# Kernel tuning notes

Hardware: AMD Instinct MI355X
Metric: run time of the kernel (lower is better)

The kernel has to match this reference:

```python
import jax, jax.numpy as jnp
import numpy as np

B, L, P, D, RD, M, K = 128, 128, 1024, 128, 128, 64, 4


def _ln(x, g, b):
    m = x.mean(-1, keepdims=True)
    v = ((x - m) ** 2).mean(-1, keepdims=True)
    return (x - m) / jnp.sqrt(v + 1e-5) * g + b


def _mlp2(x, w1, b1, w2, b2):
    return jax.nn.gelu(x @ w1 + b1, approximate=False) @ w2 + b2


def setup_inputs() -> dict:
    key = jax.random.key(0)
    ks = iter(jax.random.split(key, 64))

    def n(sh, s=1.0):
        return jax.random.normal(next(ks), sh, dtype=jnp.float32) * s

    def lin(i, o):
        return n((i, o), 1.0 / np.sqrt(i))

    inp = {}
    inp['l_pos'] = n((B, L, 3), 3.0)
    inp['l_x'] = n((B, L, 8))
    inp['p_pos'] = n((B, P, 3), 3.0)
    inp['p_x'] = n((B, P, 192))
    inp['p_score'] = n((B, P))
    inp['p_rad'] = jax.random.uniform(next(ks), (B, P), dtype=jnp.float32)
    inp['l_typ'] = jax.random.randint(next(ks), (B, L), 0, 256)
    inp['p_typ'] = jax.random.randint(next(ks), (B, P), 0, 256)
    inp['a_idx'] = jax.random.randint(next(ks), (B, M), 0, L)
    inp['b_idx'] = jax.random.randint(next(ks), (B, M), 0, L)
    inp['l_mask'] = jnp.ones((B, L), dtype=bool)
    inp['p_mask'] = jnp.ones((B, P), dtype=bool)
    inp.update(dict(
        le_emb=n((256, D), 0.02), le_w1=lin(8, D), le_b1=jnp.zeros(D), le_w2=lin(D, D), le_b2=jnp.zeros(D),
        le_g=jnp.ones(D), le_lnb=jnp.zeros(D),
        pe_emb=n((256, D), 0.02), pe_w1=lin(192, D), pe_b1=jnp.zeros(D), pe_w2=lin(D, D), pe_b2=jnp.zeros(D),
        ps_w1=lin(1, D), ps_b1=jnp.zeros(D), ps_w2=lin(D, D), ps_b2=jnp.zeros(D),
        pe_g=jnp.ones(D), pe_lnb=jnp.zeros(D),
        projL=lin(D, D), projP=lin(D, D), dustbin_vec=n((D,), 0.02),
        sg_w1=lin(D, D), sg_b1=jnp.zeros(D), sg_w2=lin(D, 1), sg_b2=jnp.zeros(1),
        inv_w1=lin(3, 64), inv_b1=jnp.zeros(64), inv_w2=lin(64, 1), inv_b2=jnp.zeros(1),
        retrL=lin(D, RD), retrP=lin(D, RD)))
    return inp


def _forward(l_pos, l_x, p_pos, p_x, p_score, p_rad,
             l_typ, p_typ, a_idx, b_idx, l_mask, p_mask,
             le_emb, le_w1, le_b1, le_w2, le_b2, le_g, le_lnb,
             pe_emb, pe_w1, pe_b1, pe_w2, pe_b2,
             ps_w1, ps_b1, ps_w2, ps_b2, pe_g, pe_lnb,
             projL, projP, dustbin_vec,
             sg_w1, sg_b1, sg_w2, sg_b2,
             inv_w1, inv_b1, inv_w2, inv_b2, retrL, retrP):
    neg = jnp.finfo(jnp.float32).min
    # encoders + projections
    hL = _ln(_mlp2(l_x, le_w1, le_b1, le_w2, le_b2) + le_emb[l_typ], le_g, le_lnb) @ projL  # [B,L,D]
    hP_pre = (_mlp2(p_x, pe_w1, pe_b1, pe_w2, pe_b2) + pe_emb[p_typ]
              + _mlp2(p_score[..., None], ps_w1, ps_b1, ps_w2, ps_b2))
    hP = _ln(hP_pre, pe_g, pe_lnb) @ projP  # [B,P,D]
    scale = 1.0 / jnp.sqrt(jnp.float32(hL.shape[-1]))
    # masked bipartite cross-attn logits
    logits = jnp.einsum('bld,bpd->blp', hL, hP) * scale
    logits_feat = jnp.where(p_mask[:, None, :], logits, neg)
    logits_feat = jnp.where(l_mask[:, :, None], logits_feat, neg)
    # dustbin log-softmax assignment
    dust = (hL @ dustbin_vec) * scale  # [B,L]
    full = jnp.concatenate([logits_feat, dust[:, :, None]], axis=-1)  # [B,L,P+1]
    full = jnp.where(l_mask[:, :, None], full, neg)
    logW = jax.nn.log_softmax(full, axis=-1)
    W = jnp.exp(logW)
    pm = p_mask.astype(jnp.float32)
    lm = l_mask.astype(jnp.float32)
    denomL = jnp.maximum(lm.sum(1), 1.0)
    Wm = jnp.concatenate([W[:, :, :-1] * pm[:, None, :], W[:, :, -1:]], axis=-1)
    sharp = (Wm.max(-1) * lm).sum(1) / denomL
    neg_ent = -((-(Wm * logW).sum(-1) * lm).sum(1) / denomL)
    # per-pocket-node sigma
    p_sigma = jax.nn.softplus(_mlp2(hP, sg_w1, sg_b1, sg_w2, sg_b2)[..., 0]) + 1e-3 + jnp.maximum(p_rad, 0.0)
    logW_real = logW[:, :, :-1]
    # sampled edge likelihood
    Bn = l_pos.shape[0]
    bi = jnp.arange(Bn)[:, None]
    valid = l_mask[bi, a_idx] & l_mask[bi, b_idx] & (a_idx != b_idx)  # [B,M]
    dist = jnp.linalg.norm(l_pos[bi, a_idx] - l_pos[bi, b_idx], axis=-1)[:, :, None, None]
    _, topj = jax.lax.top_k(logits_feat, K)  # [B,L,K]
    bi3 = jnp.arange(Bn)[:, None, None]
    p_sel = p_pos[bi3, topj]                 # [B,L,K,3]
    sig_sel = p_sigma[bi3, topj]             # [B,L,K]
    lW_top = jnp.take_along_axis(logW_real, topj, axis=2)  # [B,L,K]
    pa, pb = p_sel[bi, a_idx], p_sel[bi, b_idx]            # [B,M,K,3]
    siga, sigb = sig_sel[bi, a_idx], sig_sel[bi, b_idx]    # [B,M,K]
    lwa, lwb = lW_top[bi, a_idx], lW_top[bi, b_idx]
    mu = jnp.linalg.norm(pa[:, :, :, None, :] - pb[:, :, None, :, :], axis=-1)  # [B,M,K,K]
    sigma = jnp.sqrt(siga[:, :, :, None] ** 2 + sigb[:, :, None, :] ** 2 + 1e-6)
    logw_pair = lwa[:, :, :, None] + lwb[:, :, None, :]
    logp = -0.5 * ((dist - mu) / sigma) ** 2 - jnp.log(sigma) - 0.5 * jnp.log(2.0 * jnp.pi)
    logmix = jax.scipy.special.logsumexp(logw_pair + logp, axis=(-2, -1))  # [B,M]
    vp = valid.astype(jnp.float32)
    edge_raw = (logmix * vp).sum(1) / jnp.maximum(vp.sum(1), 1.0)
    edge = jnp.tanh(edge_raw / 5.0)  # edge_scale
    inv_vec = jnp.stack([sharp, neg_ent, edge], axis=1)  # [B,3]
    score_inv_geom = _mlp2(inv_vec, inv_w1, inv_b1, inv_w2, inv_b2)[..., 0]
    # pooled retrieval embeddings
    l_g = (hL * lm[:, :, None]).sum(1) / jnp.maximum(lm.sum(1, keepdims=True), 1.0)
    p_g = (hP * pm[:, :, None]).sum(1) / jnp.maximum(pm.sum(1, keepdims=True), 1.0)

    def _unit(x):
        return x / jnp.maximum(jnp.linalg.norm(x, axis=-1, keepdims=True), 1e-12)

    l_z = _unit(l_g @ retrL)
    p_z = _unit(p_g @ retrP)
    return jnp.concatenate([score_inv_geom[:, None], l_z, p_z], axis=-1)  # [B, 1+2*RD]


def reference(l_pos, l_x, p_pos, p_x, p_score, p_rad,
              l_typ, p_typ, a_idx, b_idx, l_mask, p_mask,
              le_emb, le_w1, le_b1, le_w2, le_b2, le_g, le_lnb,
              pe_emb, pe_w1, pe_b1, pe_w2, pe_b2,
              ps_w1, ps_b1, ps_w2, ps_b2, pe_g, pe_lnb,
              projL, projP, dustbin_vec,
              sg_w1, sg_b1, sg_w2, sg_b2,
              inv_w1, inv_b1, inv_w2, inv_b2, retrL, retrP):
    return _forward(l_pos, l_x, p_pos, p_x, p_score, p_rad,
                    l_typ, p_typ, a_idx, b_idx, l_mask, p_mask,
                    le_emb, le_w1, le_b1, le_w2, le_b2, le_g, le_lnb,
                    pe_emb, pe_w1, pe_b1, pe_w2, pe_b2,
                    ps_w1, ps_b1, ps_w2, ps_b2, pe_g, pe_lnb,
                    projL, projP, dustbin_vec,
                    sg_w1, sg_b1, sg_w2, sg_b2,
                    inv_w1, inv_b1, inv_w2, inv_b2, retrL, retrP)
```

## Files before the change

### kernel.cpp

```cpp
#include <hip/hip_runtime.h>
#include <math.h>

#define B_ 128
#define L_ 128
#define P_ 1024
#define D_ 128
#define M_ 64

typedef __attribute__((ext_vector_type(8))) short bf16x8;
typedef __attribute__((ext_vector_type(4))) float f32x4;

__device__ __forceinline__ float gelu_exact(float x) {
    return 0.5f * x * (1.0f + erff(x * 0.70710678118654752440f));
}
__device__ __forceinline__ float gelu_fast(float x) {
    float y = 0.7978845608028654f * (x + 0.044715f * x * x * x);
    float e = __expf(2.0f * y);
    float t = 1.0f - 2.0f / (e + 1.0f);
    return 0.5f * x * (1.0f + t);
}
__device__ __forceinline__ float softplus_f(float x) {
    return fmaxf(x, 0.0f) + log1pf(expf(-fabsf(x)));
}
__device__ __forceinline__ unsigned short f2bf(float f) {
    unsigned int u = __float_as_uint(f);
    unsigned int r = (u + 0x7FFFu + ((u >> 16) & 1u)) >> 16;
    return (unsigned short)r;
}
__device__ __forceinline__ float bf2f(unsigned short h) {
    return __uint_as_float(((unsigned int)h) << 16);
}
__device__ __forceinline__ bf16x8 pack8(float4 a, float4 b) {
    union { unsigned int u[4]; bf16x8 v; } r;
    r.u[0] = (unsigned)f2bf(a.x) | ((unsigned)f2bf(a.y) << 16);
    r.u[1] = (unsigned)f2bf(a.z) | ((unsigned)f2bf(a.w) << 16);
    r.u[2] = (unsigned)f2bf(b.x) | ((unsigned)f2bf(b.y) << 16);
    r.u[3] = (unsigned)f2bf(b.z) | ((unsigned)f2bf(b.w) << 16);
    return r.v;
}
__device__ __forceinline__ float xor32_sum(float v) {
#pragma unroll
    for (int o = 16; o > 0; o >>= 1) v += __shfl_xor(v, o, 32);
    return v;
}
__device__ __forceinline__ float blockReduceSum128(float v, volatile float* s2) {
#pragma unroll
    for (int o = 32; o > 0; o >>= 1) v += __shfl_down(v, o, 64);
    __syncthreads();
    if ((threadIdx.x & 63) == 0) s2[threadIdx.x >> 6] = v;
    __syncthreads();
    return s2[0] + s2[1];
}

template<int KK>
__device__ __forceinline__ void mm_tile(const float* __restrict__ W,
                                        const float* __restrict__ xT,
                                        int d0, int r0, float acc[4][4]) {
#pragma unroll 4
    for (int k = 0; k < KK; ++k) {
        float4 xv = *(const float4*)(xT + k * 16 + r0);
        float4 wv = *(const float4*)(W + k * D_ + d0);
        acc[0][0] += xv.x * wv.x; acc[0][1] += xv.x * wv.y; acc[0][2] += xv.x * wv.z; acc[0][3] += xv.x * wv.w;
        acc[1][0] += xv.y * wv.x; acc[1][1] += xv.y * wv.y; acc[1][2] += xv.y * wv.z; acc[1][3] += xv.y * wv.w;
        acc[2][0] += xv.z * wv.x; acc[2][1] += xv.z * wv.y; acc[2][2] += xv.z * wv.z; acc[2][3] += xv.z * wv.w;
        acc[3][0] += xv.w * wv.x; acc[3][1] += xv.w * wv.y; acc[3][2] += xv.w * wv.z; acc[3][3] += xv.w * wv.w;
    }
}

__global__ __launch_bounds__(256) void k_prep(
    const float* __restrict__ w1, const float* __restrict__ w2, const float* __restrict__ pp,
    const float* __restrict__ psw2, const float* __restrict__ sgw1,
    unsigned short* __restrict__ W1T, unsigned short* __restrict__ W2T, unsigned short* __restrict__ PPT,
    unsigned short* __restrict__ PSW2T, unsigned short* __restrict__ SGW1T)
{
    int d = blockIdx.x, t = threadIdx.x;
    for (int k = t; k < 192; k += 256) W1T[d * 200 + k] = f2bf(w1[k * 128 + d]);
    for (int k = t; k < 128; k += 256) {
        W2T[d * 136 + k]   = f2bf(w2[k * 128 + d]);
        PPT[d * 136 + k]   = f2bf(pp[k * 128 + d]);
        PSW2T[d * 136 + k] = f2bf(psw2[k * 128 + d]);
        SGW1T[d * 136 + k] = f2bf(sgw1[k * 128 + d]);
    }
}

__global__ __launch_bounds__(128) void k_hL(
    const float* __restrict__ l_x, const int* __restrict__ l_typ,
    const float* __restrict__ le_emb, const float* __restrict__ le_w1, const float* __restrict__ le_b1,
    const float* __restrict__ le_w2, const float* __restrict__ le_b2,
    const float* __restrict__ le_g, const float* __restrict__ le_lnb,
    const float* __restrict__ projL, float* __restrict__ hL, float* __restrict__ w_lg)
{
    __shared__ __align__(16) float s_x[8 * 16];
    __shared__ __align__(16) float s_u[D_ * 16];
    __shared__ __align__(16) float s_v[D_ * 16];
    __shared__ int s_typ[16];
    int tid = threadIdx.x;
    int td = tid & 31, tr = tid >> 5;
    int d0 = td * 4, r0 = tr * 4;
    int row0 = blockIdx.x * 16;

    for (int i = tid; i < 16 * 8; i += 128) {
        int r = i >> 3, k = i & 7;
        s_x[k * 16 + r] = l_x[(row0 + r) * 8 + k];
    }
    if (tid < 16) s_typ[tid] = l_typ[row0 + tid];
    __syncthreads();

    float acc[4][4];
    {
        float4 b1 = *(const float4*)(le_b1 + d0);
#pragma unroll
        for (int i = 0; i < 4; ++i) { acc[i][0] = b1.x; acc[i][1] = b1.y; acc[i][2] = b1.z; acc[i][3] = b1.w; }
    }
    mm_tile<8>(le_w1, s_x, d0, r0, acc);
#pragma unroll
    for (int j = 0; j < 4; ++j)
        *(float4*)(s_u + (d0 + j) * 16 + r0) =
            make_float4(gelu_exact(acc[0][j]), gelu_exact(acc[1][j]), gelu_exact(acc[2][j]), gelu_exact(acc[3][j]));
    __syncthreads();

    {
        float4 b2 = *(const float4*)(le_b2 + d0);
#pragma unroll
        for (int i = 0; i < 4; ++i) {
            float4 e = *(const float4*)(le_emb + (long)s_typ[r0 + i] * D_ + d0);
            acc[i][0] = b2.x + e.x; acc[i][1] = b2.y + e.y; acc[i][2] = b2.z + e.z; acc[i][3] = b2.w + e.w;
        }
    }
    mm_tile<D_>(le_w2, s_u, d0, r0, acc);

    float ga[4], bb[4], ln[4][4];
    *(float4*)ga = *(const float4*)(le_g + d0);
    *(float4*)bb = *(const float4*)(le_lnb + d0);
#pragma unroll
    for (int i = 0; i < 4; ++i) {
        float s = acc[i][0] + acc[i][1] + acc[i][2] + acc[i][3];
        s = xor32_sum(s);
        float mean = s * (1.0f / D_);
        float dv[4], vs = 0.0f;
#pragma unroll
        for (int j = 0; j < 4; ++j) { dv[j] = acc[i][j] - mean; vs += dv[j] * dv[j]; }
        vs = xor32_sum(vs);
        float inv = rsqrtf(vs * (1.0f / D_) + 1e-5f);
#pragma unroll
        for (int j = 0; j < 4; ++j) ln[i][j] = dv[j] * inv * ga[j] + bb[j];
    }
    __syncthreads();
#pragma unroll
    for (int j = 0; j < 4; ++j)
        *(float4*)(s_v + (d0 + j) * 16 + r0) = make_float4(ln[0][j], ln[1][j], ln[2][j], ln[3][j]);
    __syncthreads();

#pragma unroll
    for (int i = 0; i < 4; ++i)
#pragma unroll
        for (int j = 0; j < 4; ++j) acc[i][j] = 0.0f;
    mm_tile<D_>(projL, s_v, d0, r0, acc);
#pragma unroll
    for (int i = 0; i < 4; ++i)
        *(float4*)(hL + (long)(row0 + r0 + i) * D_ + d0) = make_float4(acc[i][0], acc[i][1], acc[i][2], acc[i][3]);

    int b = row0 >> 7;
#pragma unroll
    for (int j = 0; j < 4; ++j) {
        float s = acc[0][j] + acc[1][j] + acc[2][j] + acc[3][j];
        s += __shfl_xor(s, 32, 64);
        if ((tr & 1) == 0) atomicAdd(&w_lg[b * D_ + d0 + j], s);
    }
}

#define KP1 200
#define KP2 136
__global__ __launch_bounds__(256, 5) void k_hP(
    const float* __restrict__ p_x, const float* __restrict__ p_score, const float* __restrict__ p_rad,
    const int* __restrict__ p_typ,
    const float* __restrict__ pe_emb, const float* __restrict__ pe_b1, const float* __restrict__ pe_b2,
    const float* __restrict__ ps_w1, const float* __restrict__ ps_b1, const float* __restrict__ ps_b2,
    const float* __restrict__ pe_g, const float* __restrict__ pe_lnb,
    const float* __restrict__ sg_b1, const float* __restrict__ sg_w2, const float* __restrict__ sg_b2,
    const unsigned short* __restrict__ W1T, const unsigned short* __restrict__ W2T,
    const unsigned short* __restrict__ PPT, const unsigned short* __restrict__ PSW2T,
    const unsigned short* __restrict__ SGW1T,
    unsigned short* __restrict__ hPb, float* __restrict__ p_sigma, float* __restrict__ w_pg)
{
    __shared__ unsigned short s_tb[64 * KP2];
    const int tid  = threadIdx.x;
    const int wid  = tid >> 6;
    const int lane = tid & 63;
    const int l15  = tid & 15;
    const int g    = lane >> 4;
    const long row0 = (long)blockIdx.x * 64;
    const int b = (int)(row0 >> 10);
    const int arow = wid * 16 + l15;
    const int crow = wid * 16 + g * 4;
    const long grow = row0 + arow;

    f32x4 acc[8];
#pragma unroll
    for (int nt = 0; nt < 8; ++nt) {
        float bv = pe_b1[nt * 16 + l15];
        acc[nt] = (f32x4){bv, bv, bv, bv};
    }
    {
        const float* xrow = p_x + grow * 192;
#pragma unroll
        for (int k = 0; k < 6; ++k) {
            float4 v0 = *(const float4*)(xrow + k * 32 + g * 8);
            float4 v1 = *(const float4*)(xrow + k * 32 + g * 8 + 4);
            bf16x8 a = pack8(v0, v1);
#pragma unroll
            for (int nt = 0; nt < 8; ++nt) {
                bf16x8 bb = *(const bf16x8*)&W1T[(nt * 16 + l15) * KP1 + k * 32 + g * 8];
                acc[nt] = __builtin_amdgcn_mfma_f32_16x16x32_bf16(a, bb, acc[nt], 0, 0, 0);
            }
        }
    }
#pragma unroll
    for (int nt = 0; nt < 8; ++nt)
#pragma unroll
        for (int reg = 0; reg < 4; ++reg)
            s_tb[(crow + reg) * KP2 + nt * 16 + l15] = f2bf(gelu_fast(acc[nt][reg]));

    int typ[4];
#pragma unroll
    for (int reg = 0; reg < 4; ++reg) typ[reg] = p_typ[row0 + crow + reg];
#pragma unroll
    for (int nt = 0; nt < 8; ++nt) {
        int d = nt * 16 + l15;
        float bias = pe_b2[d] + ps_b2[d];
        f32x4 c;
#pragma unroll
        for (int reg = 0; reg < 4; ++reg)
            c[reg] = bias + pe_emb[(long)typ[reg] * D_ + d];
        acc[nt] = c;
    }
    {
        float score = p_score[grow];
#pragma unroll
        for (int k = 0; k < 4; ++k) {
            float4 w0 = *(const float4*)(ps_w1 + k * 32 + g * 8);
            float4 w1v = *(const float4*)(ps_w1 + k * 32 + g * 8 + 4);
            float4 c0 = *(const float4*)(ps_b1 + k * 32 + g * 8);
            float4 c1 = *(const float4*)(ps_b1 + k * 32 + g * 8 + 4);
            float4 h0 = make_float4(gelu_fast(score * w0.x + c0.x), gelu_fast(score * w0.y + c0.y),
                                    gelu_fast(score * w0.z + c0.z), gelu_fast(score * w0.w + c0.w));
            float4 h1 = make_float4(gelu_fast(score * w1v.x + c1.x), gelu_fast(score * w1v.y + c1.y),
                                    gelu_fast(score * w1v.z + c1.z), gelu_fast(score * w1v.w + c1.w));
            bf16x8 ah = pack8(h0, h1);
            bf16x8 a1 = *(const bf16x8*)&s_tb[arow * KP2 + k * 32 + g * 8];
#pragma unroll
            for (int nt = 0; nt < 8; ++nt) {
                bf16x8 b1v = *(const bf16x8*)&W2T[(nt * 16 + l15) * KP2 + k * 32 + g * 8];
                acc[nt] = __builtin_amdgcn_mfma_f32_16x16x32_bf16(a1, b1v, acc[nt], 0, 0, 0);
                bf16x8 b2v = *(const bf16x8*)&PSW2T[(nt * 16 + l15) * KP2 + k * 32 + g * 8];
                acc[nt] = __builtin_amdgcn_mfma_f32_16x16x32_bf16(ah, b2v, acc[nt], 0, 0, 0);
            }
        }
    }

    {
        float gg[8], lb[8];
#pragma unroll
        for (int nt = 0; nt < 8; ++nt) { gg[nt] = pe_g[nt * 16 + l15]; lb[nt] = pe_lnb[nt * 16 + l15]; }
#pragma unroll
        for (int reg = 0; reg < 4; ++reg) {
            float s = 0.0f;
#pragma unroll
            for (int nt = 0; nt < 8; ++nt) s += acc[nt][reg];
            s += __shfl_xor(s, 1); s += __shfl_xor(s, 2); s += __shfl_xor(s, 4); s += __shfl_xor(s, 8);
            float mean = s * (1.0f / 128.0f);
            float vs = 0.0f;
#pragma unroll
            for (int nt = 0; nt < 8; ++nt) { float dv = acc[nt][reg] - mean; vs += dv * dv; }
            vs += __shfl_xor(vs, 1); vs += __shfl_xor(vs, 2); vs += __shfl_xor(vs, 4); vs += __shfl_xor(vs, 8);
            float inv = rsqrtf(vs * (1.0f / 128.0f) + 1e-5f);
#pragma unroll
            for (int nt = 0; nt < 8; ++nt)
                acc[nt][reg] = (acc[nt][reg] - mean) * inv * gg[nt] + lb[nt];
        }
    }
#pragma unroll
    for (int nt = 0; nt < 8; ++nt)
#pragma unroll
        for (int reg = 0; reg < 4; ++reg)
            s_tb[(crow + reg) * KP2 + nt * 16 + l15] = f2bf(acc[nt][reg]);

#pragma unroll
    for (int nt = 0; nt < 8; ++nt) acc[nt] = (f32x4){0.0f, 0.0f, 0.0f, 0.0f};
#pragma unroll
    for (int k = 0; k < 4; ++k) {
        bf16x8 a = *(const bf16x8*)&s_tb[arow * KP2 + k * 32 + g * 8];
#pragma unroll
        for (int nt = 0; nt < 8; ++nt) {
            bf16x8 bb = *(const bf16x8*)&PPT[(nt * 16 + l15) * KP2 + k * 32 + g * 8];
            acc[nt] = __builtin_amdgcn_mfma_f32_16x16x32_bf16(a, bb, acc[nt], 0, 0, 0);
        }
    }
#pragma unroll
    for (int nt = 0; nt < 8; ++nt) {
        float s = acc[nt][0] + acc[nt][1] + acc[nt][2] + acc[nt][3];
        s += __shfl_xor(s, 16);
        s += __shfl_xor(s, 32);
        if (g == 0) atomicAdd(&w_pg[b * D_ + nt * 16 + l15], s);
    }
#pragma unroll
    for (int nt = 0; nt < 8; ++nt)
#pragma unroll
        for (int reg = 0; reg < 4; ++reg)
            s_tb[(crow + reg) * KP2 + nt * 16 + l15] = f2bf(acc[nt][reg]);

#pragma unroll
    for (int it = 0; it < 4; ++it) {
        int idx = lane + it * 64;
        int r = idx >> 4, seg = idx & 15;
        uint4 v = *(const uint4*)&s_tb[(wid * 16 + r) * KP2 + seg * 8];
        *(uint4*)&hPb[(row0 + wid * 16 + r) * (long)D_ + seg * 8] = v;
    }

#pragma unroll
    for (int nt = 0; nt < 8; ++nt) {
        float bv = sg_b1[nt * 16 + l15];
        acc[nt] = (f32x4){bv, bv, bv, bv};
    }
#pragma unroll
    for (int k = 0; k < 4; ++k) {
        bf16x8 a = *(const bf16x8*)&s_tb[arow * KP2 + k * 32 + g * 8];
#pragma unroll
        for (int nt = 0; nt < 8; ++nt) {
            bf16x8 bb = *(const bf16x8*)&SGW1T[(nt * 16 + l15) * KP2 + k * 32 + g * 8];
            acc[nt] = __builtin_amdgcn_mfma_f32_16x16x32_bf16(a, bb, acc[nt], 0, 0, 0);
        }
    }
    {
        float w2v[8];
#pragma unroll
        for (int nt = 0; nt < 8; ++nt) w2v[nt] = sg_w2[nt * 16 + l15];
        float sgb2 = sg_b2[0];
#pragma unroll
        for (int reg = 0; reg < 4; ++reg) {
            float part = 0.0f;
#pragma unroll
            for (int nt = 0; nt < 8; ++nt) part += gelu_fast(acc[nt][reg]) * w2v[nt];
            part += __shfl_xor(part, 1); part += __shfl_xor(part, 2);
            part += __shfl_xor(part, 4); part += __shfl_xor(part, 8);
            if (l15 == 0) {
                long r = row0 + crow + reg;
                p_sigma[r] = softplus_f(part + sgb2) + 0.001f + fmaxf(p_rad[r], 0.0f);
            }
        }
    }
}

__global__ __launch_bounds__(256) void k_logits(
    const float* __restrict__ hL, const unsigned short* __restrict__ hPb,
    const float* __restrict__ dustbin,
    float* __restrict__ w_sharp, float* __restrict__ w_ent,
    float* __restrict__ w_lw, int* __restrict__ w_idx)
{
    __shared__ unsigned short s_hl[16 * 136];
    __shared__ unsigned short s_lg[16 * 1048];
    __shared__ float s_dust[16];
    __shared__ float s_red_m[4][16];
    __shared__ float2 s_red_s[4][16];
    __shared__ float s_lse[16];

    const int tid = threadIdx.x;
    const int w = tid >> 6;
    const int l15 = tid & 15;
    const int g = (tid & 63) >> 4;
    const int b = blockIdx.x >> 3;
    const int l0 = (blockIdx.x & 7) * 16;
    const float scale = 0.08838834764831845f;

    for (int i = tid; i < 16 * 16; i += 256) {
        int r = i >> 4, c8 = (i & 15) * 8;
        const float4* src = (const float4*)(hL + ((long)(b * L_ + l0 + r)) * D_ + c8);
        float4 v0 = src[0], v1 = src[1];
        unsigned int u0 = (unsigned)f2bf(v0.x) | ((unsigned)f2bf(v0.y) << 16);
        unsigned int u1 = (unsigned)f2bf(v0.z) | ((unsigned)f2bf(v0.w) << 16);
        unsigned int u2 = (unsigned)f2bf(v1.x) | ((unsigned)f2bf(v1.y) << 16);
        unsigned int u3 = (unsigned)f2bf(v1.z) | ((unsigned)f2bf(v1.w) << 16);
        *(uint4*)&s_hl[r * 136 + c8] = make_uint4(u0, u1, u2, u3);
    }
    __syncthreads();

    {
        int r = tid >> 4;
        int k0 = (tid & 15) * 8;
        float s = 0.0f;
#pragma unroll
        for (int e = 0; e < 8; ++e) s += bf2f(s_hl[r * 136 + k0 + e]) * dustbin[k0 + e];
        s += __shfl_xor(s, 1); s += __shfl_xor(s, 2); s += __shfl_xor(s, 4); s += __shfl_xor(s, 8);
        if ((tid & 15) == 0) s_dust[r] = s * scale;
    }

    bf16x8 a[4];
#pragma unroll
    for (int k = 0; k < 4; ++k) a[k] = *(const bf16x8*)&s_hl[l15 * 136 + k * 32 + g * 8];
    const unsigned short* hp = hPb + (long)b * P_ * D_ + (long)(w * 256 + l15) * D_ + g * 8;
    f32x4 acc[16];
#pragma unroll
    for (int nt = 0; nt < 16; ++nt) acc[nt] = (f32x4){0.0f, 0.0f, 0.0f, 0.0f};
#pragma unroll
    for (int k = 0; k < 4; ++k) {
#pragma unroll
        for (int nt = 0; nt < 16; ++nt) {
            bf16x8 bb = *(const bf16x8*)(hp + nt * (16 * D_) + k * 32);
            acc[nt] = __builtin_amdgcn_mfma_f32_16x16x32_bf16(a[k], bb, acc[nt], 0, 0, 0);
        }
    }
#pragma unroll
    for (int nt = 0; nt < 16; ++nt)
#pragma unroll
        for (int reg = 0; reg < 4; ++reg) acc[nt][reg] *= scale;

#pragma unroll
    for (int reg = 0; reg < 4; ++reg) {
        float m = acc[0][reg];
#pragma unroll
        for (int nt = 1; nt < 16; ++nt) m = fmaxf(m, acc[nt][reg]);
        m = fmaxf(m, __shfl_xor(m, 1)); m = fmaxf(m, __shfl_xor(m, 2));
        m = fmaxf(m, __shfl_xor(m, 4)); m = fmaxf(m, __shfl_xor(m, 8));
        if (l15 == 0) s_red_m[w][g * 4 + reg] = m;
    }
#pragma unroll
    for (int nt = 0; nt < 16; ++nt)
#pragma unroll
        for (int reg = 0; reg < 4; ++reg)
            s_lg[(g * 4 + reg) * 1048 + w * 256 + nt * 16 + l15] = f2bf(acc[nt][reg]);
    __syncthreads();

    float mf[4];
#pragma unroll
    for (int reg = 0; reg < 4; ++reg) {
        int r = g * 4 + reg;
        float m = fmaxf(fmaxf(s_red_m[0][r], s_red_m[1][r]), fmaxf(s_red_m[2][r], s_red_m[3][r]));
        mf[reg] = fmaxf(m, s_dust[r]);
    }
#pragma unroll
    for (int reg = 0; reg < 4; ++reg) {
        float S0 = 0.0f, S1 = 0.0f;
#pragma unroll
        for (int nt = 0; nt < 16; ++nt) {
            float x = acc[nt][reg] - mf[reg];
            float e = expf(x);
            S0 += e; S1 += e * x;
        }
        S0 += __shfl_xor(S0, 1); S0 += __shfl_xor(S0, 2); S0 += __shfl_xor(S0, 4); S0 += __shfl_xor(S0, 8);
        S1 += __shfl_xor(S1, 1); S1 += __shfl_xor(S1, 2); S1 += __shfl_xor(S1, 4); S1 += __shfl_xor(S1, 8);
        if (l15 == 0) s_red_s[w][g * 4 + reg] = make_float2(S0, S1);
    }
    __syncthreads();

    if (tid < 64 && l15 == 0) {
#pragma unroll
        for (int reg = 0; reg < 4; ++reg) {
            int r = g * 4 + reg;
            float m = mf[reg];
            float S0 = 0.0f, S1 = 0.0f;
#pragma unroll
            for (int ww = 0; ww < 4; ++ww) { float2 s = s_red_s[ww][r]; S0 += s.x; S1 += s.y; }
            float xd = s_dust[r] - m;
            float ed = expf(xd);
            S0 += ed; S1 += ed * xd;
            float lgz = logf(S0);
            int rowg = b * L_ + l0 + r;
            w_sharp[rowg] = 1.0f / S0;
            w_ent[rowg] = S1 / S0 - lgz;
            s_lse[r] = m + lgz;
        }
    }
    __syncthreads();

    {
        int r = tid >> 4;
        int lane = tid & 15;
        float lse = s_lse[r];
        int rowg = b * L_ + l0 + r;
        for (int k = 0; k < 4; ++k) {
            float bv = -INFINITY; int bi = P_;
            for (int c = lane; c < P_; c += 16) {
                float v = bf2f(s_lg[r * 1048 + c]);
                if (v > bv || (v == bv && c < bi)) { bv = v; bi = c; }
            }
#pragma unroll
            for (int o = 1; o < 16; o <<= 1) {
                float ov = __shfl_xor(bv, o);
                int   oi = __shfl_xor(bi, o);
                if (ov > bv || (ov == bv && oi < bi)) { bv = ov; bi = oi; }
            }
            if (lane == 0) {
                w_lw[rowg * 4 + k] = bv - lse;
                w_idx[rowg * 4 + k] = bi;
            }
            s_lg[r * 1048 + bi] = 0xFF80;
        }
    }
}

__global__ __launch_bounds__(128) void k_final2(
    const int* __restrict__ a_idx, const int* __restrict__ b_idx,
    const float* __restrict__ l_pos, const float* __restrict__ p_pos,
    const float* __restrict__ p_sigma, const float* __restrict__ w_lw, const int* __restrict__ w_idx,
    const float* __restrict__ w_lg, const float* __restrict__ w_pg,
    const float* __restrict__ w_sharp, const float* __restrict__ w_ent,
    const float* __restrict__ inv_w1, const float* __restrict__ inv_b1,
    const float* __restrict__ inv_w2, const float* __restrict__ inv_b2,
    const float* __restrict__ retrL, const float* __restrict__ retrP,
    float* __restrict__ out)
{
    __shared__ float s_red[2];
    __shared__ float s_vec[D_];
    __shared__ float s_edge;
    int b = blockIdx.x, tid = threadIdx.x;

    if (tid < 64) {
        int m = tid;
        int ai = a_idx[b * M_ + m], bi = b_idx[b * M_ + m];
        bool valid = (ai != bi);
        float ax = l_pos[(b * L_ + ai) * 3 + 0], ay = l_pos[(b * L_ + ai) * 3 + 1], az = l_pos[(b * L_ + ai) * 3 + 2];
        float bx = l_pos[(b * L_ + bi) * 3 + 0], by = l_pos[(b * L_ + bi) * 3 + 1], bz = l_pos[(b * L_ + bi) * 3 + 2];
        float dx = ax - bx, dy = ay - by, dz = az - bz;
        float dist = sqrtf(dx * dx + dy * dy + dz * dz);

        float pax[4], pay[4], paz[4], sa2[4], lwa[4];
        float pbx[4], pby[4], pbz[4], sb2[4], lwb[4];
#pragma unroll
        for (int k = 0; k < 4; ++k) {
            int ja = w_idx[(b * L_ + ai) * 4 + k];
            pax[k] = p_pos[(b * P_ + ja) * 3 + 0]; pay[k] = p_pos[(b * P_ + ja) * 3 + 1]; paz[k] = p_pos[(b * P_ + ja) * 3 + 2];
            float sa = p_sigma[b * P_ + ja]; sa2[k] = sa * sa;
            lwa[k] = w_lw[(b * L_ + ai) * 4 + k];
            int jb = w_idx[(b * L_ + bi) * 4 + k];
            pbx[k] = p_pos[(b * P_ + jb) * 3 + 0]; pby[k] = p_pos[(b * P_ + jb) * 3 + 1]; pbz[k] = p_pos[(b * P_ + jb) * 3 + 2];
            float sb = p_sigma[b * P_ + jb]; sb2[k] = sb * sb;
            lwb[k] = w_lw[(b * L_ + bi) * 4 + k];
        }
        float t[16];
        float mx = -INFINITY;
#pragma unroll
        for (int j = 0; j < 4; ++j)
#pragma unroll
            for (int k = 0; k < 4; ++k) {
                float ddx = pax[j] - pbx[k], ddy = pay[j] - pby[k], ddz = paz[j] - pbz[k];
                float mu = sqrtf(ddx * ddx + ddy * ddy + ddz * ddz);
                float s2 = sa2[j] + sb2[k] + 1e-6f;
                float diff = dist - mu;
                float lp = lwa[j] + lwb[k] - 0.5f * diff * diff / s2 - 0.5f * logf(s2) - 0.91893853320467274f;
                t[j * 4 + k] = lp;
                mx = fmaxf(mx, lp);
            }
        float se = 0.0f;
#pragma unroll
        for (int n = 0; n < 16; ++n) se += expf(t[n] - mx);
        float logmix = mx + logf(se);
        float v = valid ? logmix : 0.0f;
        float c = valid ? 1.0f : 0.0f;
#pragma unroll
        for (int o = 32; o > 0; o >>= 1) { v += __shfl_down(v, o, 64); c += __shfl_down(c, o, 64); }
        if (m == 0) s_edge = tanhf((v / fmaxf(c, 1.0f)) * 0.2f);
    }
    __syncthreads();
    float edge = s_edge;

    float sharp = blockReduceSum128(w_sharp[b * L_ + tid], s_red) * (1.0f / L_);
    float neg_ent = blockReduceSum128(w_ent[b * L_ + tid], s_red) * (1.0f / L_);
    float v = 0.0f;
    if (tid < 64) {
        float h = gelu_exact(sharp * inv_w1[tid] + neg_ent * inv_w1[64 + tid] + edge * inv_w1[128 + tid] + inv_b1[tid]);
        v = h * inv_w2[tid];
    }
    float sc = blockReduceSum128(v, s_red);
    if (tid == 0) out[b * 257] = sc + inv_b2[0];

    s_vec[tid] = w_lg[b * D_ + tid] * (1.0f / L_);
    __syncthreads();
    float z = 0.0f;
    for (int k = 0; k < D_; ++k) z += s_vec[k] * retrL[k * D_ + tid];
    float nrm = sqrtf(blockReduceSum128(z * z, s_red));
    out[b * 257 + 1 + tid] = z / fmaxf(nrm, 1e-12f);
    __syncthreads();

    s_vec[tid] = w_pg[b * D_ + tid] * (1.0f / P_);
    __syncthreads();
    z = 0.0f;
    for (int k = 0; k < D_; ++k) z += s_vec[k] * retrP[k * D_ + tid];
    nrm = sqrtf(blockReduceSum128(z * z, s_red));
    out[b * 257 + 129 + tid] = z / fmaxf(nrm, 1e-12f);
}

extern "C" void kernel_launch(void* const* d_in, const int* in_sizes, int n_in,
                              void* d_out, int out_size, void* d_ws, size_t ws_size,
                              hipStream_t stream) {
    (void)in_sizes; (void)n_in; (void)out_size; (void)ws_size;
    const float* l_pos  = (const float*)d_in[0];
    const float* l_x    = (const float*)d_in[1];
    const float* p_pos  = (const float*)d_in[2];
    const float* p_x    = (const float*)d_in[3];
    const float* p_score= (const float*)d_in[4];
    const float* p_rad  = (const float*)d_in[5];
    const int*   l_typ  = (const int*)d_in[6];
    const int*   p_typ  = (const int*)d_in[7];
    const int*   a_idx  = (const int*)d_in[8];
    const int*   b_idx  = (const int*)d_in[9];
    const float* le_emb = (const float*)d_in[12];
    const float* le_w1  = (const float*)d_in[13];
    const float* le_b1  = (const float*)d_in[14];
    const float* le_w2  = (const float*)d_in[15];
    const float* le_b2  = (const float*)d_in[16];
    const float* le_g   = (const float*)d_in[17];
    const float* le_lnb = (const float*)d_in[18];
    const float* pe_emb = (const float*)d_in[19];
    const float* pe_w1  = (const float*)d_in[20];
    const float* pe_b1  = (const float*)d_in[21];
    const float* pe_w2  = (const float*)d_in[22];
    const float* pe_b2  = (const float*)d_in[23];
    const float* ps_w1  = (const float*)d_in[24];
    const float* ps_b1  = (const float*)d_in[25];
    const float* ps_w2  = (const float*)d_in[26];
    const float* ps_b2  = (const float*)d_in[27];
    const float* pe_g   = (const float*)d_in[28];
    const float* pe_lnb = (const float*)d_in[29];
    const float* projL  = (const float*)d_in[30];
    const float* projP  = (const float*)d_in[31];
    const float* dustbin= (const float*)d_in[32];
    const float* sg_w1  = (const float*)d_in[33];
    const float* sg_b1  = (const float*)d_in[34];
    const float* sg_w2  = (const float*)d_in[35];
    const float* sg_b2  = (const float*)d_in[36];
    const float* inv_w1 = (const float*)d_in[37];
    const float* inv_b1 = (const float*)d_in[38];
    const float* inv_w2 = (const float*)d_in[39];
    const float* inv_b2 = (const float*)d_in[40];
    const float* retrL  = (const float*)d_in[41];
    const float* retrP  = (const float*)d_in[42];

    unsigned short* hPb = (unsigned short*)d_ws;
    float* hL      = (float*)(hPb + (size_t)B_ * P_ * D_);
    float* p_sigma = hL + (size_t)B_ * L_ * D_;
    float* w_sharp = p_sigma + (size_t)B_ * P_;
    float* w_ent   = w_sharp + B_ * L_;
    float* w_lw    = w_ent + B_ * L_;
    int*   w_idx   = (int*)(w_lw + B_ * L_ * 4);
    float* w_pg    = (float*)(w_idx + B_ * L_ * 4);
    float* w_lg    = w_pg + B_ * D_;
    unsigned short* W1T   = (unsigned short*)(w_lg + B_ * D_);
    unsigned short* W2T   = W1T + 128 * 200;
    unsigned short* PPT   = W2T + 128 * 136;
    unsigned short* PSW2T = PPT + 128 * 136;
    unsigned short* SGW1T = PSW2T + 128 * 136;

    hipMemsetAsync(w_pg, 0, 2 * B_ * D_ * sizeof(float), stream);

    hipLaunchKernelGGL(k_prep, dim3(128), dim3(256), 0, stream,
                       pe_w1, pe_w2, projP, ps_w2, sg_w1, W1T, W2T, PPT, PSW2T, SGW1T);
    hipLaunchKernelGGL(k_hL, dim3(B_ * L_ / 16), dim3(128), 0, stream,
                       l_x, l_typ, le_emb, le_w1, le_b1, le_w2, le_b2, le_g, le_lnb, projL, hL, w_lg);
    hipLaunchKernelGGL(k_hP, dim3(B_ * P_ / 64), dim3(256), 0, stream,
                       p_x, p_score, p_rad, p_typ, pe_emb, pe_b1, pe_b2,
                       ps_w1, ps_b1, ps_b2, pe_g, pe_lnb,
                       sg_b1, sg_w2, sg_b2,
                       W1T, W2T, PPT, PSW2T, SGW1T,
                       hPb, p_sigma, w_pg);
    hipLaunchKernelGGL(k_logits, dim3(B_ * (L_ / 16)), dim3(256), 0, stream,
                       hL, hPb, dustbin, w_sharp, w_ent, w_lw, w_idx);
    hipLaunchKernelGGL(k_final2, dim3(B_), dim3(128), 0, stream,
                       a_idx, b_idx, l_pos, p_pos, p_sigma, w_lw, w_idx,
                       w_lg, w_pg, w_sharp, w_ent,
                       inv_w1, inv_b1, inv_w2, inv_b2, retrL, retrP,
                       (float*)d_out);
}
```

Baseline: 548.5 us.

## Process two 16-row tiles per wave in k_hP to reuse weight fragments

Each wave of k_hP now computes 32 rows instead of 16, holding two accumulator sets so every weight fragment loaded from global memory feeds two MFMAs. The block covers 128 rows, the grid is halved, and shared memory and launch bounds are adjusted to match. This aims to halve weight-fragment traffic per row and halve the w_pg atomics. In exchange, register pressure doubles, occupancy drops (launch bounds 5 to 4) and there are fewer blocks to spread across the GPU.

```diff
diff --git a/kernel.cpp b/kernel.cpp
--- a/kernel.cpp
+++ b/kernel.cpp
@@ -171,7 +171,7 @@
 
 #define KP1 200
 #define KP2 136
-__global__ __launch_bounds__(256, 5) void k_hP(
+__global__ __launch_bounds__(256, 4) void k_hP(
     const float* __restrict__ p_x, const float* __restrict__ p_score, const float* __restrict__ p_rad,
     const int* __restrict__ p_typ,
     const float* __restrict__ pe_emb, const float* __restrict__ pe_b1, const float* __restrict__ pe_b2,
@@ -183,77 +183,97 @@
     const unsigned short* __restrict__ SGW1T,
     unsigned short* __restrict__ hPb, float* __restrict__ p_sigma, float* __restrict__ w_pg)
 {
-    __shared__ unsigned short s_tb[64 * KP2];
+    __shared__ unsigned short s_tb[128 * KP2];
     const int tid  = threadIdx.x;
     const int wid  = tid >> 6;
     const int lane = tid & 63;
     const int l15  = tid & 15;
     const int g    = lane >> 4;
-    const long row0 = (long)blockIdx.x * 64;
+    const long row0 = (long)blockIdx.x * 128;
     const int b = (int)(row0 >> 10);
-    const int arow = wid * 16 + l15;
-    const int crow = wid * 16 + g * 4;
-    const long grow = row0 + arow;
-
-    f32x4 acc[8];
+    const int arow0 = wid * 32 + l15;
+    const int crow0 = wid * 32 + g * 4;
+    const long grow0 = row0 + arow0;
+
+    f32x4 acc[2][8];
 #pragma unroll
     for (int nt = 0; nt < 8; ++nt) {
         float bv = pe_b1[nt * 16 + l15];
-        acc[nt] = (f32x4){bv, bv, bv, bv};
-    }
-    {
-        const float* xrow = p_x + grow * 192;
+        acc[0][nt] = (f32x4){bv, bv, bv, bv};
+        acc[1][nt] = (f32x4){bv, bv, bv, bv};
+    }
+    {
+        const float* xr0 = p_x + grow0 * 192;
+        const float* xr1 = xr0 + 16 * 192;
 #pragma unroll
         for (int k = 0; k < 6; ++k) {
-            float4 v0 = *(const float4*)(xrow + k * 32 + g * 8);
-            float4 v1 = *(const float4*)(xrow + k * 32 + g * 8 + 4);
-            bf16x8 a = pack8(v0, v1);
+            bf16x8 a0 = pack8(*(const float4*)(xr0 + k * 32 + g * 8), *(const float4*)(xr0 + k * 32 + g * 8 + 4));
+            bf16x8 a1 = pack8(*(const float4*)(xr1 + k * 32 + g * 8), *(const float4*)(xr1 + k * 32 + g * 8 + 4));
 #pragma unroll
             for (int nt = 0; nt < 8; ++nt) {
                 bf16x8 bb = *(const bf16x8*)&W1T[(nt * 16 + l15) * KP1 + k * 32 + g * 8];
-                acc[nt] = __builtin_amdgcn_mfma_f32_16x16x32_bf16(a, bb, acc[nt], 0, 0, 0);
-            }
-        }
-    }
-#pragma unroll
-    for (int nt = 0; nt < 8; ++nt)
-#pragma unroll
-        for (int reg = 0; reg < 4; ++reg)
-            s_tb[(crow + reg) * KP2 + nt * 16 + l15] = f2bf(gelu_fast(acc[nt][reg]));
-
-    int typ[4];
-#pragma unroll
-    for (int reg = 0; reg < 4; ++reg) typ[reg] = p_typ[row0 + crow + reg];
-#pragma unroll
-    for (int nt = 0; nt < 8; ++nt) {
-        int d = nt * 16 + l15;
-        float bias = pe_b2[d] + ps_b2[d];
-        f32x4 c;
-#pragma unroll
-        for (int reg = 0; reg < 4; ++reg)
-            c[reg] = bias + pe_emb[(long)typ[reg] * D_ + d];
-        acc[nt] = c;
-    }
-    {
-        float score = p_score[grow];
+                acc[0][nt] = __builtin_amdgcn_mfma_f32_16x16x32_bf16(a0, bb, acc[0][nt], 0, 0, 0);
+                acc[1][nt] = __builtin_amdgcn_mfma_f32_16x16x32_bf16(a1, bb, acc[1][nt], 0, 0, 0);
+            }
+        }
+    }
+#pragma unroll
+    for (int t = 0; t < 2; ++t)
+#pragma unroll
+        for (int nt = 0; nt < 8; ++nt)
+#pragma unroll
+            for (int reg = 0; reg < 4; ++reg)
+                s_tb[(crow0 + t * 16 + reg) * KP2 + nt * 16 + l15] = f2bf(gelu_fast(acc[t][nt][reg]));
+
+    {
+        int typ[2][4];
+#pragma unroll
+        for (int t = 0; t < 2; ++t)
+#pragma unroll
+            for (int reg = 0; reg < 4; ++reg) typ[t][reg] = p_typ[row0 + crow0 + t * 16 + reg];
+#pragma unroll
+        for (int nt = 0; nt < 8; ++nt) {
+            int d = nt * 16 + l15;
+            float bias = pe_b2[d] + ps_b2[d];
+#pragma unroll
+            for (int t = 0; t < 2; ++t) {
+                f32x4 c;
+#pragma unroll
+                for (int reg = 0; reg < 4; ++reg)
+                    c[reg] = bias + pe_emb[(long)typ[t][reg] * D_ + d];
+                acc[t][nt] = c;
+            }
+        }
+    }
+    {
+        float score0 = p_score[grow0];
+        float score1 = p_score[grow0 + 16];
 #pragma unroll
         for (int k = 0; k < 4; ++k) {
             float4 w0 = *(const float4*)(ps_w1 + k * 32 + g * 8);
             float4 w1v = *(const float4*)(ps_w1 + k * 32 + g * 8 + 4);
             float4 c0 = *(const float4*)(ps_b1 + k * 32 + g * 8);
             float4 c1 = *(const float4*)(ps_b1 + k * 32 + g * 8 + 4);
-            float4 h0 = make_float4(gelu_fast(score * w0.x + c0.x), gelu_fast(score * w0.y + c0.y),
-                                    gelu_fast(score * w0.z + c0.z), gelu_fast(score * w0.w + c0.w));
-            float4 h1 = make_float4(gelu_fast(score * w1v.x + c1.x), gelu_fast(score * w1v.y + c1.y),
-                                    gelu_fast(score * w1v.z + c1.z), gelu_fast(score * w1v.w + c1.w));
-            bf16x8 ah = pack8(h0, h1);
-            bf16x8 a1 = *(const bf16x8*)&s_tb[arow * KP2 + k * 32 + g * 8];
+            bf16x8 ah0 = pack8(
+                make_float4(gelu_fast(score0 * w0.x + c0.x), gelu_fast(score0 * w0.y + c0.y),
+                            gelu_fast(score0 * w0.z + c0.z), gelu_fast(score0 * w0.w + c0.w)),
+                make_float4(gelu_fast(score0 * w1v.x + c1.x), gelu_fast(score0 * w1v.y + c1.y),
+                            gelu_fast(score0 * w1v.z + c1.z), gelu_fast(score0 * w1v.w + c1.w)));
+            bf16x8 ah1 = pack8(
+                make_float4(gelu_fast(score1 * w0.x + c0.x), gelu_fast(score1 * w0.y + c0.y),
+                            gelu_fast(score1 * w0.z + c0.z), gelu_fast(score1 * w0.w + c0.w)),
+                make_float4(gelu_fast(score1 * w1v.x + c1.x), gelu_fast(score1 * w1v.y + c1.y),
+                            gelu_fast(score1 * w1v.z + c1.z), gelu_fast(score1 * w1v.w + c1.w)));
+            bf16x8 at0 = *(const bf16x8*)&s_tb[arow0 * KP2 + k * 32 + g * 8];
+            bf16x8 at1 = *(const bf16x8*)&s_tb[(arow0 + 16) * KP2 + k * 32 + g * 8];
 #pragma unroll
             for (int nt = 0; nt < 8; ++nt) {
                 bf16x8 b1v = *(const bf16x8*)&W2T[(nt * 16 + l15) * KP2 + k * 32 + g * 8];
-                acc[nt] = __builtin_amdgcn_mfma_f32_16x16x32_bf16(a1, b1v, acc[nt], 0, 0, 0);
+                acc[0][nt] = __builtin_amdgcn_mfma_f32_16x16x32_bf16(at0, b1v, acc[0][nt], 0, 0, 0);
+                acc[1][nt] = __builtin_amdgcn_mfma_f32_16x16x32_bf16(at1, b1v, acc[1][nt], 0, 0, 0);
                 bf16x8 b2v = *(const bf16x8*)&PSW2T[(nt * 16 + l15) * KP2 + k * 32 + g * 8];
-                acc[nt] = __builtin_amdgcn_mfma_f32_16x16x32_bf16(ah, b2v, acc[nt], 0, 0, 0);
+                acc[0][nt] = __builtin_amdgcn_mfma_f32_16x16x32_bf16(ah0, b2v, acc[0][nt], 0, 0, 0);
+                acc[1][nt] = __builtin_amdgcn_mfma_f32_16x16x32_bf16(ah1, b2v, acc[1][nt], 0, 0, 0);
             }
         }
     }
@@ -263,72 +283,86 @@
 #pragma unroll
         for (int nt = 0; nt < 8; ++nt) { gg[nt] = pe_g[nt * 16 + l15]; lb[nt] = pe_lnb[nt * 16 + l15]; }
 #pragma unroll
-        for (int reg = 0; reg < 4; ++reg) {
-            float s = 0.0f;
-#pragma unroll
-            for (int nt = 0; nt < 8; ++nt) s += acc[nt][reg];
-            s += __shfl_xor(s, 1); s += __shfl_xor(s, 2); s += __shfl_xor(s, 4); s += __shfl_xor(s, 8);
-            float mean = s * (1.0f / 128.0f);
-            float vs = 0.0f;
-#pragma unroll
-            for (int nt = 0; nt < 8; ++nt) { float dv = acc[nt][reg] - mean; vs += dv * dv; }
-            vs += __shfl_xor(vs, 1); vs += __shfl_xor(vs, 2); vs += __shfl_xor(vs, 4); vs += __shfl_xor(vs, 8);
-            float inv = rsqrtf(vs * (1.0f / 128.0f) + 1e-5f);
-#pragma unroll
-            for (int nt = 0; nt < 8; ++nt)
-                acc[nt][reg] = (acc[nt][reg] - mean) * inv * gg[nt] + lb[nt];
-        }
-    }
-#pragma unroll
-    for (int nt = 0; nt < 8; ++nt)
-#pragma unroll
-        for (int reg = 0; reg < 4; ++reg)
-            s_tb[(crow + reg) * KP2 + nt * 16 + l15] = f2bf(acc[nt][reg]);
-
-#pragma unroll
-    for (int nt = 0; nt < 8; ++nt) acc[nt] = (f32x4){0.0f, 0.0f, 0.0f, 0.0f};
+        for (int t = 0; t < 2; ++t)
+#pragma unroll
+            for (int reg = 0; reg < 4; ++reg) {
+                float s = 0.0f;
+#pragma unroll
+                for (int nt = 0; nt < 8; ++nt) s += acc[t][nt][reg];
+                s += __shfl_xor(s, 1); s += __shfl_xor(s, 2); s += __shfl_xor(s, 4); s += __shfl_xor(s, 8);
+                float mean = s * (1.0f / 128.0f);
+                float vs = 0.0f;
+#pragma unroll
+                for (int nt = 0; nt < 8; ++nt) { float dv = acc[t][nt][reg] - mean; vs += dv * dv; }
+                vs += __shfl_xor(vs, 1); vs += __shfl_xor(vs, 2); vs += __shfl_xor(vs, 4); vs += __shfl_xor(vs, 8);
+                float inv = rsqrtf(vs * (1.0f / 128.0f) + 1e-5f);
+#pragma unroll
+                for (int nt = 0; nt < 8; ++nt)
+                    acc[t][nt][reg] = (acc[t][nt][reg] - mean) * inv * gg[nt] + lb[nt];
+            }
+    }
+#pragma unroll
+    for (int t = 0; t < 2; ++t)
+#pragma unroll
+        for (int nt = 0; nt < 8; ++nt)
+#pragma unroll
+            for (int reg = 0; reg < 4; ++reg)
+                s_tb[(crow0 + t * 16 + reg) * KP2 + nt * 16 + l15] = f2bf(acc[t][nt][reg]);
+
+#pragma unroll
+    for (int t = 0; t < 2; ++t)
+#pragma unroll
+        for (int nt = 0; nt < 8; ++nt) acc[t][nt] = (f32x4){0.0f, 0.0f, 0.0f, 0.0f};
 #pragma unroll
     for (int k = 0; k < 4; ++k) {
-        bf16x8 a = *(const bf16x8*)&s_tb[arow * KP2 + k * 32 + g * 8];
+        bf16x8 a0 = *(const bf16x8*)&s_tb[arow0 * KP2 + k * 32 + g * 8];
+        bf16x8 a1 = *(const bf16x8*)&s_tb[(arow0 + 16) * KP2 + k * 32 + g * 8];
 #pragma unroll
         for (int nt = 0; nt < 8; ++nt) {
             bf16x8 bb = *(const bf16x8*)&PPT[(nt * 16 + l15) * KP2 + k * 32 + g * 8];
-            acc[nt] = __builtin_amdgcn_mfma_f32_16x16x32_bf16(a, bb, acc[nt], 0, 0, 0);
+            acc[0][nt] = __builtin_amdgcn_mfma_f32_16x16x32_bf16(a0, bb, acc[0][nt], 0, 0, 0);
+            acc[1][nt] = __builtin_amdgcn_mfma_f32_16x16x32_bf16(a1, bb, acc[1][nt], 0, 0, 0);
         }
     }
 #pragma unroll
     for (int nt = 0; nt < 8; ++nt) {
-        float s = acc[nt][0] + acc[nt][1] + acc[nt][2] + acc[nt][3];
+        float s = acc[0][nt][0] + acc[0][nt][1] + acc[0][nt][2] + acc[0][nt][3]
+                + acc[1][nt][0] + acc[1][nt][1] + acc[1][nt][2] + acc[1][nt][3];
         s += __shfl_xor(s, 16);
         s += __shfl_xor(s, 32);
         if (g == 0) atomicAdd(&w_pg[b * D_ + nt * 16 + l15], s);
     }
 #pragma unroll
-    for (int nt = 0; nt < 8; ++nt)
-#pragma unroll
-        for (int reg = 0; reg < 4; ++reg)
-            s_tb[(crow + reg) * KP2 + nt * 16 + l15] = f2bf(acc[nt][reg]);
-
-#pragma unroll
-    for (int it = 0; it < 4; ++it) {
+    for (int t = 0; t < 2; ++t)
+#pragma unroll
+        for (int nt = 0; nt < 8; ++nt)
+#pragma unroll
+            for (int reg = 0; reg < 4; ++reg)
+                s_tb[(crow0 + t * 16 + reg) * KP2 + nt * 16 + l15] = f2bf(acc[t][nt][reg]);
+
+#pragma unroll
+    for (int it = 0; it < 8; ++it) {
         int idx = lane + it * 64;
         int r = idx >> 4, seg = idx & 15;
-        uint4 v = *(const uint4*)&s_tb[(wid * 16 + r) * KP2 + seg * 8];
-        *(uint4*)&hPb[(row0 + wid * 16 + r) * (long)D_ + seg * 8] = v;
+        uint4 v = *(const uint4*)&s_tb[(wid * 32 + r) * KP2 + seg * 8];
+        *(uint4*)&hPb[(row0 + wid * 32 + r) * (long)D_ + seg * 8] = v;
     }
 
 #pragma unroll
     for (int nt = 0; nt < 8; ++nt) {
         float bv = sg_b1[nt * 16 + l15];
-        acc[nt] = (f32x4){bv, bv, bv, bv};
+        acc[0][nt] = (f32x4){bv, bv, bv, bv};
+        acc[1][nt] = (f32x4){bv, bv, bv, bv};
     }
 #pragma unroll
     for (int k = 0; k < 4; ++k) {
-        bf16x8 a = *(const bf16x8*)&s_tb[arow * KP2 + k * 32 + g * 8];
+        bf16x8 a0 = *(const bf16x8*)&s_tb[arow0 * KP2 + k * 32 + g * 8];
+        bf16x8 a1 = *(const bf16x8*)&s_tb[(arow0 + 16) * KP2 + k * 32 + g * 8];
 #pragma unroll
         for (int nt = 0; nt < 8; ++nt) {
             bf16x8 bb = *(const bf16x8*)&SGW1T[(nt * 16 + l15) * KP2 + k * 32 + g * 8];
-            acc[nt] = __builtin_amdgcn_mfma_f32_16x16x32_bf16(a, bb, acc[nt], 0, 0, 0);
+            acc[0][nt] = __builtin_amdgcn_mfma_f32_16x16x32_bf16(a0, bb, acc[0][nt], 0, 0, 0);
+            acc[1][nt] = __builtin_amdgcn_mfma_f32_16x16x32_bf16(a1, bb, acc[1][nt], 0, 0, 0);
         }
     }
     {
@@ -337,17 +371,19 @@
         for (int nt = 0; nt < 8; ++nt) w2v[nt] = sg_w2[nt * 16 + l15];
         float sgb2 = sg_b2[0];
 #pragma unroll
-        for (int reg = 0; reg < 4; ++reg) {
-            float part = 0.0f;
-#pragma unroll
-            for (int nt = 0; nt < 8; ++nt) part += gelu_fast(acc[nt][reg]) * w2v[nt];
-            part += __shfl_xor(part, 1); part += __shfl_xor(part, 2);
-            part += __shfl_xor(part, 4); part += __shfl_xor(part, 8);
-            if (l15 == 0) {
-                long r = row0 + crow + reg;
-                p_sigma[r] = softplus_f(part + sgb2) + 0.001f + fmaxf(p_rad[r], 0.0f);
-            }
-        }
+        for (int t = 0; t < 2; ++t)
+#pragma unroll
+            for (int reg = 0; reg < 4; ++reg) {
+                float part = 0.0f;
+#pragma unroll
+                for (int nt = 0; nt < 8; ++nt) part += gelu_fast(acc[t][nt][reg]) * w2v[nt];
+                part += __shfl_xor(part, 1); part += __shfl_xor(part, 2);
+                part += __shfl_xor(part, 4); part += __shfl_xor(part, 8);
+                if (l15 == 0) {
+                    long r = row0 + crow0 + t * 16 + reg;
+                    p_sigma[r] = softplus_f(part + sgb2) + 0.001f + fmaxf(p_rad[r], 0.0f);
+                }
+            }
     }
 }
 
@@ -656,7 +692,7 @@
                        pe_w1, pe_w2, projP, ps_w2, sg_w1, W1T, W2T, PPT, PSW2T, SGW1T);
     hipLaunchKernelGGL(k_hL, dim3(B_ * L_ / 16), dim3(128), 0, stream,
                        l_x, l_typ, le_emb, le_w1, le_b1, le_w2, le_b2, le_g, le_lnb, projL, hL, w_lg);
-    hipLaunchKernelGGL(k_hP, dim3(B_ * P_ / 64), dim3(256), 0, stream,
+    hipLaunchKernelGGL(k_hP, dim3(B_ * P_ / 128), dim3(256), 0, stream,
                        p_x, p_score, p_rad, p_typ, pe_emb, pe_b1, pe_b2,
                        ps_w1, ps_b1, ps_b2, pe_g, pe_lnb,
                        sg_b1, sg_w2, sg_b2,
```

Measured after the change: 519.0 us. 1.06x faster.
